# Kernel optimization log

Hardware: AMD Instinct MI355X
Metric: run time of the kernel (lower is better)

Reference implementation:

```python
import math
import jax, jax.numpy as jnp
import numpy as np

OLEN = 512
RATIO = 0.5
DROP_P = 0.2


def _gat(x, src, dst, W, a_s, a_d, b):
    """PyG GATConv (heads=1, concat=True, add_self_loops=True, neg_slope=0.2)."""
    n = x.shape[0]
    loops = jnp.arange(n, dtype=src.dtype)
    s = jnp.concatenate([src, loops])  # [E+N] source nodes
    d = jnp.concatenate([dst, loops])  # [E+N] destination nodes
    h = x @ W                           # [N, H]
    alpha_s = h @ a_s                   # [N]
    alpha_d = h @ a_d                   # [N]
    e = jax.nn.leaky_relu(alpha_s[s] + alpha_d[d], 0.2)  # [E+N]
    # segment softmax over destination neighborhoods
    m = jax.ops.segment_max(e, d, num_segments=n)
    ee = jnp.exp(e - m[d])
    denom = jax.ops.segment_sum(ee, d, num_segments=n)
    alpha = ee / denom[d]
    out = jax.ops.segment_sum(alpha[:, None] * h[s], d, num_segments=n)
    return out + b


def _forward(x, src, dst, W1, a_src1, a_dst1, b1, W2, a_src2, a_dst2, b2,
             W3, a_src3, a_dst3, b3, W_rel, W_root, b_pool):
    N, E = x.shape[0], src.shape[0]
    key = jax.random.key(42)
    h = x
    for i, (W, a_s, a_d, b) in enumerate([(W1, a_src1, a_dst1, b1),
                                          (W2, a_src2, a_dst2, b2),
                                          (W3, a_src3, a_dst3, b3)]):
        h = jax.nn.relu(_gat(h, src, dst, W, a_s, a_d, b))
        keep = jax.random.bernoulli(jax.random.fold_in(key, i), 1.0 - DROP_P, h.shape)
        h = jnp.where(keep, h / (1.0 - DROP_P), 0.0)  # F.dropout(training=True)

    # SAGPooling(GraphConv score, ratio=0.5, tanh) repeated until n <= 512.
    # Node counts are static per iteration (k = ceil(0.5*n)); edge arrays keep
    # fixed size E with a validity mask (edges dropped when an endpoint is pooled away).
    cur_src, cur_dst = src, dst
    emask = jnp.ones((E,), dtype=h.dtype)
    n = N
    while True:
        agg = jax.ops.segment_sum(h[cur_src] * emask[:, None], cur_dst, num_segments=n)
        score = (agg @ W_rel + h @ W_root + b_pool)[:, 0]  # GraphConv(d->1), aggr='add'
        score = jnp.tanh(score)
        k = math.ceil(RATIO * n)
        top_vals, perm = jax.lax.top_k(score, k)
        h = h[perm] * top_vals[:, None]
        inv = jnp.full((n,), -1, dtype=cur_src.dtype).at[perm].set(
            jnp.arange(k, dtype=cur_src.dtype))
        ns, nd = inv[cur_src], inv[cur_dst]
        valid = (ns >= 0) & (nd >= 0)
        emask = emask * valid.astype(emask.dtype)
        cur_src = jnp.where(valid, ns, 0)
        cur_dst = jnp.where(valid, nd, 0)
        n = k
        if n <= OLEN:
            break

    out = jnp.zeros((OLEN, h.shape[1]), h.dtype).at[:n].set(h)
    return out


def setup_inputs() -> dict:
    key = jax.random.key(0)
    ks = jax.random.split(key, 20)
    N, E, IDIM, HDIM = 50000, 800000, 128, 200
    inp = {
        "x": jax.random.normal(ks[0], (N, IDIM), jnp.float32),
        "src": jax.random.randint(ks[1], (E,), 0, N, jnp.int32),
        "dst": jax.random.randint(ks[2], (E,), 0, N, jnp.int32),
    }
    def w(k, shape, fan_in):
        return jax.random.normal(k, shape, jnp.float32) / np.sqrt(fan_in).astype(np.float32)
    inp["W1"] = w(ks[3], (IDIM, HDIM), IDIM)
    inp["a_src1"] = w(ks[4], (HDIM,), HDIM)
    inp["a_dst1"] = w(ks[5], (HDIM,), HDIM)
    inp["b1"] = jnp.zeros((HDIM,), jnp.float32)
    inp["W2"] = w(ks[6], (HDIM, HDIM), HDIM)
    inp["a_src2"] = w(ks[7], (HDIM,), HDIM)
    inp["a_dst2"] = w(ks[8], (HDIM,), HDIM)
    inp["b2"] = jnp.zeros((HDIM,), jnp.float32)
    inp["W3"] = w(ks[9], (HDIM, HDIM), HDIM)
    inp["a_src3"] = w(ks[10], (HDIM,), HDIM)
    inp["a_dst3"] = w(ks[11], (HDIM,), HDIM)
    inp["b3"] = jnp.zeros((HDIM,), jnp.float32)
    inp["W_rel"] = w(ks[12], (HDIM, 1), HDIM)
    inp["W_root"] = w(ks[13], (HDIM, 1), HDIM)
    inp["b_pool"] = jnp.zeros((1,), jnp.float32)
    return inp


def reference(x, src, dst, W1, a_src1, a_dst1, b1, W2, a_src2, a_dst2, b2,
              W3, a_src3, a_dst3, b3, W_rel, W_root, b_pool):
    return _forward(x, src, dst, W1, a_src1, a_dst1, b1, W2, a_src2, a_dst2, b2,
                    W3, a_src3, a_dst3, b3, W_rel, W_root, b_pool)
```

## Files before the change

kernel.cpp:

```cpp
#include <hip/hip_runtime.h>
#include <cstdint>
#include <cstddef>


__host__ __device__ inline void tf_round(uint32_t &x0, uint32_t &x1, int r) {
  x0 += x1;
  x1 = (x1 << r) | (x1 >> (32 - r));
  x1 ^= x0;
}

__host__ __device__ inline void threefry2x32(uint32_t k0, uint32_t k1,
                                             uint32_t &x0, uint32_t &x1) {
  uint32_t ks2 = k0 ^ k1 ^ 0x1BD11BDAu;
  x0 += k0; x1 += k1;
  tf_round(x0, x1, 13); tf_round(x0, x1, 15); tf_round(x0, x1, 26); tf_round(x0, x1, 6);
  x0 += k1; x1 += ks2 + 1u;
  tf_round(x0, x1, 17); tf_round(x0, x1, 29); tf_round(x0, x1, 16); tf_round(x0, x1, 24);
  x0 += ks2; x1 += k0 + 2u;
  tf_round(x0, x1, 13); tf_round(x0, x1, 15); tf_round(x0, x1, 26); tf_round(x0, x1, 6);
  x0 += k0; x1 += k1 + 3u;
  tf_round(x0, x1, 17); tf_round(x0, x1, 29); tf_round(x0, x1, 16); tf_round(x0, x1, 24);
  x0 += k1; x1 += ks2 + 4u;
  tf_round(x0, x1, 13); tf_round(x0, x1, 15); tf_round(x0, x1, 26); tf_round(x0, x1, 6);
  x0 += ks2; x1 += k0 + 5u;
}

__global__ __launch_bounds__(256) void gemm200_k(
    const float* __restrict__ A, const float* __restrict__ B,
    float* __restrict__ C, int M, int K) {
  __shared__ __align__(16) float As[128 * 8];
  __shared__ __align__(16) float Bs[8][208];
  int tid = threadIdx.x;
  int m0 = blockIdx.x * 128;
  int r = tid >> 2;
  int colBase = (tid & 3) * 52;
  float acc0[52], acc1[52];
#pragma unroll
  for (int q = 0; q < 52; q++) { acc0[q] = 0.f; acc1[q] = 0.f; }

  for (int k0 = 0; k0 < K; k0 += 8) {
    {
      int row = tid >> 1;
      int c = (tid & 1) * 4;
      int gm = m0 + row;
      float4 v = make_float4(0.f, 0.f, 0.f, 0.f);
      if (gm < M) v = *(const float4*)(A + (size_t)gm * K + (k0 + c));
      *(float4*)(&As[row * 8 + c]) = v;
    }
    for (int t = tid; t < 400; t += 256) {
      int kk = t / 50;
      int c = (t - kk * 50) * 4;
      *(float4*)(&Bs[kk][c]) = *(const float4*)(B + (size_t)(k0 + kk) * 200 + c);
    }
    __syncthreads();
#pragma unroll
    for (int kk = 0; kk < 8; kk++) {
      float a0 = As[r * 8 + kk];
      float a1 = As[(r + 64) * 8 + kk];
#pragma unroll
      for (int q = 0; q < 13; q++) {
        float4 b = *(const float4*)(&Bs[kk][colBase + 4 * q]);
        acc0[4 * q + 0] += a0 * b.x; acc0[4 * q + 1] += a0 * b.y;
        acc0[4 * q + 2] += a0 * b.z; acc0[4 * q + 3] += a0 * b.w;
        acc1[4 * q + 0] += a1 * b.x; acc1[4 * q + 1] += a1 * b.y;
        acc1[4 * q + 2] += a1 * b.z; acc1[4 * q + 3] += a1 * b.w;
      }
    }
    __syncthreads();
  }
  int gm0 = m0 + r, gm1 = m0 + r + 64;
#pragma unroll
  for (int q = 0; q < 52; q++) {
    int col = colBase + q;
    if (col < 200) {
      if (gm0 < M) C[(size_t)gm0 * 200 + col] = acc0[q];
      if (gm1 < M) C[(size_t)gm1 * 200 + col] = acc1[q];
    }
  }
}

__global__ __launch_bounds__(256) void dual_dot_k(
    const float* __restrict__ H, const float* __restrict__ v1,
    const float* __restrict__ v2, float* __restrict__ o1,
    float* __restrict__ o2, int n) {
  int wave = blockIdx.x * 4 + (threadIdx.x >> 6);
  int lane = threadIdx.x & 63;
  if (wave >= n) return;
  const float* row = H + (size_t)wave * 200;
  float s1 = 0.f, s2 = 0.f;
  for (int d = lane; d < 200; d += 64) {
    float h = row[d];
    s1 += h * v1[d];
    s2 += h * v2[d];
  }
  for (int off = 32; off; off >>= 1) {
    s1 += __shfl_down(s1, off);
    s2 += __shfl_down(s2, off);
  }
  if (lane == 0) { o1[wave] = s1; o2[wave] = s2; }
}

__global__ __launch_bounds__(256) void indeg_k(const int* __restrict__ dst,
                                               int* __restrict__ cnt, int E) {
  int e = blockIdx.x * 256 + threadIdx.x;
  if (e < E) atomicAdd(&cnt[dst[e]], 1);
}

__global__ __launch_bounds__(256) void scan_k(const int* __restrict__ cnt,
                                              int* __restrict__ rowptr, int N) {
  __shared__ int psum[256];
  int t = threadIdx.x;
  int CH = (N + 255) / 256;
  int beg = t * CH, end = min(beg + CH, N);
  if (beg > N) { beg = N; }
  int s = 0;
  for (int i = beg; i < end; i++) s += cnt[i];
  psum[t] = s;
  __syncthreads();
  if (t == 0) {
    int run = 0;
    for (int i = 0; i < 256; i++) { int v = psum[i]; psum[i] = run; run += v; }
  }
  __syncthreads();
  int run = psum[t];
  for (int i = beg; i < end; i++) { rowptr[i] = run; run += cnt[i]; }
  if (end == N && beg <= N) rowptr[N] = run;
}

__global__ __launch_bounds__(256) void cpyint_k(const int* __restrict__ a,
                                                int* __restrict__ b, int n) {
  int i = blockIdx.x * 256 + threadIdx.x;
  if (i < n) b[i] = a[i];
}

__global__ __launch_bounds__(256) void place_k(const int* __restrict__ dst,
                                               int* __restrict__ curs,
                                               int* __restrict__ csr, int E) {
  int e = blockIdx.x * 256 + threadIdx.x;
  if (e >= E) return;
  int pos = atomicAdd(&curs[dst[e]], 1);
  csr[pos] = e;
}

__global__ __launch_bounds__(256) void sortrow_k(const int* __restrict__ rowptr,
                                                 int* __restrict__ csr, int N) {
  int d = blockIdx.x * 256 + threadIdx.x;
  if (d >= N) return;
  int b = rowptr[d], e2 = rowptr[d + 1];
  for (int i = b + 1; i < e2; i++) {
    int v = csr[i];
    int j = i - 1;
    while (j >= b && csr[j] > v) { csr[j + 1] = csr[j]; j--; }
    csr[j + 1] = v;
  }
}

__device__ inline float dec_ord(unsigned enc) {
  unsigned b = (enc & 0x80000000u) ? (enc ^ 0x80000000u) : ~enc;
  return __uint_as_float(b);
}

__global__ __launch_bounds__(256) void edge_max_k(
    const int* __restrict__ src, const int* __restrict__ dst,
    const float* __restrict__ as_, const float* __restrict__ ad_,
    unsigned* __restrict__ menc, int E, int N) {
  int j = blockIdx.x * 256 + threadIdx.x;
  if (j >= E + N) return;
  int s, d;
  if (j < E) { s = src[j]; d = dst[j]; } else { s = j - E; d = s; }
  float v = as_[s] + ad_[d];
  float ev = (v >= 0.f) ? v : 0.2f * v;
  unsigned b = __float_as_uint(ev);
  unsigned enc = (b & 0x80000000u) ? ~b : (b | 0x80000000u);
  atomicMax(&menc[d], enc);
}

__global__ __launch_bounds__(256) void ee_k(
    const int* __restrict__ src, const int* __restrict__ dst,
    const float* __restrict__ as_, const float* __restrict__ ad_,
    const unsigned* __restrict__ menc, float* __restrict__ ee, int E, int N) {
  int j = blockIdx.x * 256 + threadIdx.x;
  if (j >= E + N) return;
  int s, d;
  if (j < E) { s = src[j]; d = dst[j]; } else { s = j - E; d = s; }
  float v = as_[s] + ad_[d];
  float ev = (v >= 0.f) ? v : 0.2f * v;
  ee[j] = expf(ev - dec_ord(menc[d]));
}

__global__ __launch_bounds__(256) void den_k(const int* __restrict__ rowptr,
                                             const int* __restrict__ csr,
                                             const float* __restrict__ ee,
                                             float* __restrict__ den, int E, int N) {
  int d = blockIdx.x * 256 + threadIdx.x;
  if (d >= N) return;
  float s = 0.f;
  int b = rowptr[d], e2 = rowptr[d + 1];
  for (int i = b; i < e2; i++) s = __fadd_rn(s, ee[csr[i]]);
  s = __fadd_rn(s, ee[E + d]);
  den[d] = s;
}

__global__ __launch_bounds__(256) void alpha_k(const int* __restrict__ dst,
                                               const float* __restrict__ den,
                                               float* __restrict__ ee, int E, int N) {
  int j = blockIdx.x * 256 + threadIdx.x;
  if (j >= E + N) return;
  int d = (j < E) ? dst[j] : (j - E);
  ee[j] = ee[j] / den[d];
}

__global__ __launch_bounds__(256) void gat_out_k(
    const int* __restrict__ rowptr, const int* __restrict__ csr,
    const int* __restrict__ src, const float* __restrict__ alpha,
    const float* __restrict__ HW, float* __restrict__ OUT, int E, int N) {
  int node = blockIdx.x * 4 + (threadIdx.x >> 6);
  int lane = threadIdx.x & 63;
  if (node >= N || lane >= 50) return;
  int b = rowptr[node];
  int deg = rowptr[node + 1] - b;
  int cnt = deg + 1;

  auto fetchS = [&](int t, int &s, float &w) {
    if (t < deg) {
      int e = csr[b + t];
      s = src[e];
      w = alpha[e];
    } else if (t == deg) {
      s = node;
      w = alpha[E + node];
    } else {
      s = node;
      w = 0.f;
    }
  };

  int s0, s1, s2;
  float w0, w1, w2;
  fetchS(0, s0, w0);
  fetchS(1, s1, w1);
  fetchS(2, s2, w2);
  float4 h0 = *(const float4*)(HW + (size_t)s0 * 200 + 4 * lane);
  float4 h1 = *(const float4*)(HW + (size_t)s1 * 200 + 4 * lane);
  float4 acc = make_float4(0.f, 0.f, 0.f, 0.f);
  for (int t = 0; t < cnt; t++) {
    int s3;
    float w3;
    fetchS(t + 3, s3, w3);
    float4 h2 = *(const float4*)(HW + (size_t)s2 * 200 + 4 * lane);
    acc.x = __fadd_rn(acc.x, __fmul_rn(w0, h0.x));
    acc.y = __fadd_rn(acc.y, __fmul_rn(w0, h0.y));
    acc.z = __fadd_rn(acc.z, __fmul_rn(w0, h0.z));
    acc.w = __fadd_rn(acc.w, __fmul_rn(w0, h0.w));
    h0 = h1; h1 = h2;
    w0 = w1; w1 = w2; w2 = w3;
    s2 = s3;
  }
  *(float4*)(OUT + (size_t)node * 200 + 4 * lane) = acc;
}

__global__ __launch_bounds__(256) void epi_k(float* __restrict__ H,
                                             const float* __restrict__ bias,
                                             uint32_t k0, uint32_t k1, int total) {
  int t = blockIdx.x * 256 + threadIdx.x;
  if (t >= total) return;
  uint32_t x0 = 0u, x1 = (uint32_t)t;
  threefry2x32(k0, k1, x0, x1);
  uint32_t bits = x0 ^ x1;
  float u = __uint_as_float((bits >> 9) | 0x3f800000u) - 1.0f;
  int col = t % 200;
  float v = H[t] + bias[col];
  v = fmaxf(v, 0.f);
  H[t] = (u < 0.8f) ? (v / 0.8f) : 0.f;
}

__global__ __launch_bounds__(256) void einit_k(
    const int* __restrict__ src, const int* __restrict__ dst,
    int* __restrict__ cs, int* __restrict__ cd, int* __restrict__ orig,
    int E, int N) {
  int e = blockIdx.x * 256 + threadIdx.x;
  if (e < E) { cs[e] = src[e]; cd[e] = dst[e]; }
  if (e < N) orig[e] = e;
}

__global__ __launch_bounds__(256) void pool_agg_k(
    const int* __restrict__ rowptr, const int* __restrict__ csr,
    const int* __restrict__ csrc, const int* __restrict__ orig,
    const float* __restrict__ H, float* __restrict__ AGG, int n) {
  int node = blockIdx.x * 4 + (threadIdx.x >> 6);
  int lane = threadIdx.x & 63;
  if (node >= n || lane >= 50) return;
  int o = orig[node];
  int b = rowptr[o];
  int deg = rowptr[o + 1] - b;

  auto fetchS = [&](int t, int &s, float &w) {
    if (t < deg) {
      int e = csr[b + t];
      int sv = csrc[e];
      s = (sv >= 0) ? sv : 0;
      w = (sv >= 0) ? 1.f : 0.f;
    } else {
      s = 0;
      w = 0.f;
    }
  };

  int s0, s1, s2;
  float w0, w1, w2;
  fetchS(0, s0, w0);
  fetchS(1, s1, w1);
  fetchS(2, s2, w2);
  float4 h0 = *(const float4*)(H + (size_t)s0 * 200 + 4 * lane);
  float4 h1 = *(const float4*)(H + (size_t)s1 * 200 + 4 * lane);
  float4 acc = make_float4(0.f, 0.f, 0.f, 0.f);
  for (int t = 0; t < deg; t++) {
    int s3;
    float w3;
    fetchS(t + 3, s3, w3);
    float4 h2 = *(const float4*)(H + (size_t)s2 * 200 + 4 * lane);
    acc.x = __fadd_rn(acc.x, __fmul_rn(w0, h0.x));
    acc.y = __fadd_rn(acc.y, __fmul_rn(w0, h0.y));
    acc.z = __fadd_rn(acc.z, __fmul_rn(w0, h0.z));
    acc.w = __fadd_rn(acc.w, __fmul_rn(w0, h0.w));
    h0 = h1; h1 = h2;
    w0 = w1; w1 = w2; w2 = w3;
    s2 = s3;
  }
  *(float4*)(AGG + (size_t)node * 200 + 4 * lane) = acc;
}

__global__ __launch_bounds__(256) void score2_k(
    const float* __restrict__ AGG, const float* __restrict__ H,
    const float* __restrict__ wrel, const float* __restrict__ wroot,
    const float* __restrict__ bp, float* __restrict__ score, int n) {
  int node = blockIdx.x * 4 + (threadIdx.x >> 6);
  int lane = threadIdx.x & 63;
  if (node >= n) return;
  const float* arow = AGG + (size_t)node * 200;
  const float* hrow = H + (size_t)node * 200;
  float s1 = 0.f, s2 = 0.f;
  for (int d = lane; d < 200; d += 64) {
    s1 += arow[d] * wrel[d];
    s2 += hrow[d] * wroot[d];
  }
  for (int off = 32; off; off >>= 1) {
    s1 += __shfl_down(s1, off);
    s2 += __shfl_down(s2, off);
  }
  if (lane == 0) score[node] = tanhf((s1 + s2) + bp[0]);
}

__global__ __launch_bounds__(256) void renc_k(const float* __restrict__ score,
                                              unsigned* __restrict__ keyA,
                                              int* __restrict__ payA, int n) {
  int i = blockIdx.x * 256 + threadIdx.x;
  if (i >= n) return;
  unsigned b = __float_as_uint(score[i]);
  if (b == 0x80000000u) b = 0u;
  unsigned enc = (b & 0x80000000u) ? ~b : (b | 0x80000000u);
  keyA[i] = ~enc;
  payA[i] = i;
}

__global__ __launch_bounds__(256) void rhist_k(const unsigned* __restrict__ key,
                                               int* __restrict__ counts,
                                               int n, int NB, int shift) {
  __shared__ int hist[256];
  hist[threadIdx.x] = 0;
  __syncthreads();
  int i = blockIdx.x * 256 + threadIdx.x;
  if (i < n) atomicAdd(&hist[(key[i] >> shift) & 255u], 1);
  __syncthreads();
  counts[threadIdx.x * NB + blockIdx.x] = hist[threadIdx.x];
}

__global__ __launch_bounds__(256) void rscan_k(const int* __restrict__ counts,
                                               int* __restrict__ base, int NB) {
  __shared__ int tot[256];
  int t = threadIdx.x;
  int s = 0;
  for (int b = 0; b < NB; b++) s += counts[t * NB + b];
  tot[t] = s;
  __syncthreads();
  if (t == 0) {
    int run = 0;
    for (int i = 0; i < 256; i++) { int v = tot[i]; tot[i] = run; run += v; }
  }
  __syncthreads();
  int run = tot[t];
  for (int b = 0; b < NB; b++) { base[t * NB + b] = run; run += counts[t * NB + b]; }
}

__global__ __launch_bounds__(256) void rscatter_k(
    const unsigned* __restrict__ keyIn, const int* __restrict__ payIn,
    const int* __restrict__ base, unsigned* __restrict__ keyOut,
    int* __restrict__ payOut, int n, int NB, int shift) {
  __shared__ int dig[256];
  int t = threadIdx.x;
  int i = blockIdx.x * 256 + t;
  unsigned k = 0u;
  int p = 0, d = -1;
  if (i < n) {
    k = keyIn[i];
    p = payIn[i];
    d = (int)((k >> shift) & 255u);
  }
  dig[t] = d;
  __syncthreads();
  if (i < n) {
    int local = 0;
    for (int j = 0; j < t; j++) local += (dig[j] == d) ? 1 : 0;
    int pos = base[d * NB + blockIdx.x] + local;
    keyOut[pos] = k;
    payOut[pos] = p;
  }
}

__global__ __launch_bounds__(256) void ranksort_k(const int* __restrict__ pay,
                                                  int* __restrict__ perm,
                                                  int* __restrict__ inv,
                                                  int n, int k) {
  int r = blockIdx.x * 256 + threadIdx.x;
  if (r >= n) return;
  int i = pay[r];
  if (r < k) { perm[r] = i; inv[i] = r; }
  else inv[i] = -1;
}

__global__ __launch_bounds__(256) void orig_update_k(const int* __restrict__ perm,
                                                     const int* __restrict__ oin,
                                                     int* __restrict__ oout, int k) {
  int r = blockIdx.x * 256 + threadIdx.x;
  if (r < k) oout[r] = oin[perm[r]];
}

__global__ __launch_bounds__(256) void gather_k(
    const float* __restrict__ H, const int* __restrict__ perm,
    const float* __restrict__ score, float* __restrict__ Ho, int k) {
  int r = blockIdx.x;
  int d = threadIdx.x;
  int p = perm[r];
  float s = score[p];
  if (d < 200) Ho[(size_t)r * 200 + d] = __fmul_rn(H[(size_t)p * 200 + d], s);
}

__global__ __launch_bounds__(256) void remap_k(int* __restrict__ cs,
                                               int* __restrict__ cd,
                                               const int* __restrict__ inv, int E) {
  int e = blockIdx.x * 256 + threadIdx.x;
  if (e >= E) return;
  int a = cs[e];
  if (a < 0) return;
  int na = inv[a], nb = inv[cd[e]];
  bool valid = (na >= 0) && (nb >= 0);
  cs[e] = valid ? na : -1;
  cd[e] = valid ? nb : -1;
}

__global__ __launch_bounds__(256) void out_copy_k(const float* __restrict__ h,
                                                  float* __restrict__ out, int cnt) {
  int t = blockIdx.x * 256 + threadIdx.x;
  if (t < cnt) out[t] = h[t];
}

extern "C" void kernel_launch(void* const* d_in, const int* in_sizes, int n_in,
                              void* d_out, int out_size, void* d_ws, size_t ws_size,
                              hipStream_t stream) {
  const int ID = 128, HD = 200;
  const int N = in_sizes[0] / ID;
  const int E = in_sizes[1];
  const int ET = E + N;
  const int total = N * HD;

  const float* x = (const float*)d_in[0];
  const int* src = (const int*)d_in[1];
  const int* dst = (const int*)d_in[2];
  const float* W[3]   = {(const float*)d_in[3], (const float*)d_in[7], (const float*)d_in[11]};
  const float* asv[3] = {(const float*)d_in[4], (const float*)d_in[8], (const float*)d_in[12]};
  const float* adv[3] = {(const float*)d_in[5], (const float*)d_in[9], (const float*)d_in[13]};
  const float* bv[3]  = {(const float*)d_in[6], (const float*)d_in[10], (const float*)d_in[14]};
  const float* Wrel  = (const float*)d_in[15];
  const float* Wroot = (const float*)d_in[16];
  const float* bpool = (const float*)d_in[17];

  char* ws = (char*)d_ws;
  float*    bufA  = (float*)(ws + 0);
  float*    bufB  = (float*)(ws + 40000000);
  float*    as_   = (float*)(ws + 80000000);
  float*    ad_   = (float*)(ws + 80200000);
  float*    ee_   = (float*)(ws + 80400000);
  unsigned* menc  = (unsigned*)(ws + 83800000);
  float*    den   = (float*)(ws + 84000000);
  float*    score = (float*)(ws + 84200000);
  int*      rank_ = (int*)(ws + 84400000);
  int*      perm_ = (int*)(ws + 84600000);
  int*      inv_  = (int*)(ws + 84800000);
  int*      origA = (int*)(ws + 85000000);
  int*      origB = (int*)(ws + 85200000);
  int*      rowptr= (int*)(ws + 85400000);
  int*      curs  = (int*)(ws + 85650000);
  int*      csr   = (int*)(ws + 85850000);
  int*      csrc  = (int*)(ws + 89050000);
  int*      cdst  = (int*)(ws + 92250000);

  char* rx = ws + 80400000;
  unsigned* keyA   = (unsigned*)(rx + 0 * 262144);
  unsigned* keyB   = (unsigned*)(rx + 1 * 262144);
  int*      payA   = (int*)(rx + 2 * 262144);
  int*      payB   = (int*)(rx + 3 * 262144);
  int*      rcounts= (int*)(rx + 4 * 262144);
  int*      rbase  = (int*)(rx + 5 * 262144);

  uint32_t fk0[3], fk1[3];
  for (int i = 0; i < 3; i++) {
    uint32_t a = 0u, b = (uint32_t)i;
    threefry2x32(0u, 42u, a, b);
    fk0[i] = a; fk1[i] = b;
  }

  const int B256 = 256;
  hipMemsetAsync(rank_, 0, (size_t)N * 4, stream);
  indeg_k<<<(E + 255) / 256, B256, 0, stream>>>(dst, rank_, E);
  scan_k<<<1, B256, 0, stream>>>(rank_, rowptr, N);
  cpyint_k<<<(N + 255) / 256, B256, 0, stream>>>(rowptr, curs, N);
  place_k<<<(E + 255) / 256, B256, 0, stream>>>(dst, curs, csr, E);
  sortrow_k<<<(N + 255) / 256, B256, 0, stream>>>(rowptr, csr, N);

  for (int i = 0; i < 3; i++) {
    const float* in = (i == 0) ? x : bufB;
    int K = (i == 0) ? ID : HD;
    gemm200_k<<<(N + 127) / 128, B256, 0, stream>>>(in, W[i], bufA, N, K);
    dual_dot_k<<<(N + 3) / 4, B256, 0, stream>>>(bufA, asv[i], adv[i], as_, ad_, N);
    hipMemsetAsync(menc, 0, (size_t)N * 4, stream);
    edge_max_k<<<(ET + 255) / 256, B256, 0, stream>>>(src, dst, as_, ad_, menc, E, N);
    ee_k<<<(ET + 255) / 256, B256, 0, stream>>>(src, dst, as_, ad_, menc, ee_, E, N);
    den_k<<<(N + 255) / 256, B256, 0, stream>>>(rowptr, csr, ee_, den, E, N);
    alpha_k<<<(ET + 255) / 256, B256, 0, stream>>>(dst, den, ee_, E, N);
    gat_out_k<<<(N + 3) / 4, B256, 0, stream>>>(rowptr, csr, src, ee_, bufA, bufB, E, N);
    epi_k<<<(total + 255) / 256, B256, 0, stream>>>(bufB, bv[i], fk0[i], fk1[i], total);
  }

  einit_k<<<(E + 255) / 256, B256, 0, stream>>>(src, dst, csrc, cdst, origA, E, N);
  float* hcur = bufB;
  float* hnext = bufA;
  int* ocur = origA;
  int* onext = origB;
  int n = N;
  while (true) {
    int k = (n + 1) / 2;
    int NB = (n + 255) / 256;
    pool_agg_k<<<(n + 3) / 4, B256, 0, stream>>>(rowptr, csr, csrc, ocur, hcur, hnext, n);
    score2_k<<<(n + 3) / 4, B256, 0, stream>>>(hnext, hcur, Wrel, Wroot, bpool, score, n);
    renc_k<<<NB, B256, 0, stream>>>(score, keyA, payA, n);
    unsigned* ki = keyA; unsigned* ko = keyB;
    int* pi = payA; int* po = payB;
    for (int pass = 0; pass < 4; pass++) {
      int shift = pass * 8;
      rhist_k<<<NB, B256, 0, stream>>>(ki, rcounts, n, NB, shift);
      rscan_k<<<1, B256, 0, stream>>>(rcounts, rbase, NB);
      rscatter_k<<<NB, B256, 0, stream>>>(ki, pi, rbase, ko, po, n, NB, shift);
      { unsigned* t = ki; ki = ko; ko = t; }
      { int* t = pi; pi = po; po = t; }
    }
    ranksort_k<<<NB, B256, 0, stream>>>(pi, perm_, inv_, n, k);
    orig_update_k<<<(k + 255) / 256, B256, 0, stream>>>(perm_, ocur, onext, k);
    gather_k<<<k, B256, 0, stream>>>(hcur, perm_, score, hnext, k);
    remap_k<<<(E + 255) / 256, B256, 0, stream>>>(csrc, cdst, inv_, E);
    { float* t = hcur; hcur = hnext; hnext = t; }
    { int* t = ocur; ocur = onext; onext = t; }
    n = k;
    if (n <= 512) break;
  }

  hipMemsetAsync(d_out, 0, (size_t)out_size * 4, stream);
  out_copy_k<<<(n * HD + 255) / 256, B256, 0, stream>>>(hcur, (float*)d_out, n * HD);
}
```

Baseline: 3.055 ms.

## Prefetch GEMM tiles into registers, vectorize stores, and fuse radix sort stages

The GEMM now loads the next A/B k-slice into registers while computing the current one, pads the A shared tile to stride 9 to avoid bank conflicts, and writes results with float4 stores. The pooling top-k radix sort fuses key encoding with the first histogram, and fuses the final scatter with the perm/inv construction and orig-index update. This removes several kernel launches per pooling iteration and some global round trips. Register pressure in the GEMM rises from holding the prefetched tiles.

```diff
diff --git a/kernel.cpp b/kernel.cpp
--- a/kernel.cpp
+++ b/kernel.cpp
@@ -28,35 +28,50 @@
 __global__ __launch_bounds__(256) void gemm200_k(
     const float* __restrict__ A, const float* __restrict__ B,
     float* __restrict__ C, int M, int K) {
-  __shared__ __align__(16) float As[128 * 8];
+  __shared__ float As[128 * 9];
   __shared__ __align__(16) float Bs[8][208];
   int tid = threadIdx.x;
   int m0 = blockIdx.x * 128;
   int r = tid >> 2;
   int colBase = (tid & 3) * 52;
+  int nq = (colBase == 156) ? 11 : 13;
   float acc0[52], acc1[52];
 #pragma unroll
   for (int q = 0; q < 52; q++) { acc0[q] = 0.f; acc1[q] = 0.f; }
 
+  int arow = tid >> 1;
+  int ac = (tid & 1) * 4;
+  int gmA = m0 + arow;
+  const float* Aptr = A + (size_t)gmA * K + ac;
+  int bk0 = tid / 50, bc0 = (tid - bk0 * 50) * 4;
+  int t2 = tid + 256;
+  int bk1 = t2 / 50, bc1 = (t2 - bk1 * 50) * 4;
+  bool hasB1 = (t2 < 400);
+
+  float4 va = make_float4(0.f, 0.f, 0.f, 0.f);
+  if (gmA < M) va = *(const float4*)(Aptr);
+  float4 vb0 = *(const float4*)(B + (size_t)bk0 * 200 + bc0);
+  float4 vb1 = make_float4(0.f, 0.f, 0.f, 0.f);
+  if (hasB1) vb1 = *(const float4*)(B + (size_t)bk1 * 200 + bc1);
+
   for (int k0 = 0; k0 < K; k0 += 8) {
-    {
-      int row = tid >> 1;
-      int c = (tid & 1) * 4;
-      int gm = m0 + row;
-      float4 v = make_float4(0.f, 0.f, 0.f, 0.f);
-      if (gm < M) v = *(const float4*)(A + (size_t)gm * K + (k0 + c));
-      *(float4*)(&As[row * 8 + c]) = v;
+    As[arow * 9 + ac + 0] = va.x;
+    As[arow * 9 + ac + 1] = va.y;
+    As[arow * 9 + ac + 2] = va.z;
+    As[arow * 9 + ac + 3] = va.w;
+    *(float4*)(&Bs[bk0][bc0]) = vb0;
+    if (hasB1) *(float4*)(&Bs[bk1][bc1]) = vb1;
+    __syncthreads();
+    int kn = k0 + 8;
+    if (kn < K) {
+      if (gmA < M) va = *(const float4*)(Aptr + kn);
+      vb0 = *(const float4*)(B + (size_t)(kn + bk0) * 200 + bc0);
+      if (hasB1) vb1 = *(const float4*)(B + (size_t)(kn + bk1) * 200 + bc1);
     }
-    for (int t = tid; t < 400; t += 256) {
-      int kk = t / 50;
-      int c = (t - kk * 50) * 4;
-      *(float4*)(&Bs[kk][c]) = *(const float4*)(B + (size_t)(k0 + kk) * 200 + c);
-    }
-    __syncthreads();
 #pragma unroll
     for (int kk = 0; kk < 8; kk++) {
-      float a0 = As[r * 8 + kk];
-      float a1 = As[(r + 64) * 8 + kk];
+      float a0 = As[r * 9 + kk];
+      float a1 = As[(r + 64) * 9 + kk];
 #pragma unroll
       for (int q = 0; q < 13; q++) {
         float4 b = *(const float4*)(&Bs[kk][colBase + 4 * q]);
@@ -70,11 +85,15 @@
   }
   int gm0 = m0 + r, gm1 = m0 + r + 64;
 #pragma unroll
-  for (int q = 0; q < 52; q++) {
-    int col = colBase + q;
-    if (col < 200) {
-      if (gm0 < M) C[(size_t)gm0 * 200 + col] = acc0[q];
-      if (gm1 < M) C[(size_t)gm1 * 200 + col] = acc1[q];
+  for (int q = 0; q < 13; q++) {
+    if (q < nq) {
+      int col = colBase + 4 * q;
+      float4 v0 = make_float4(acc0[4 * q + 0], acc0[4 * q + 1],
+                              acc0[4 * q + 2], acc0[4 * q + 3]);
+      float4 v1 = make_float4(acc1[4 * q + 0], acc1[4 * q + 1],
+                              acc1[4 * q + 2], acc1[4 * q + 3]);
+      if (gm0 < M) *(float4*)(C + (size_t)gm0 * 200 + col) = v0;
+      if (gm1 < M) *(float4*)(C + (size_t)gm1 * 200 + col) = v1;
     }
   }
 }
@@ -351,16 +370,27 @@
   if (lane == 0) score[node] = tanhf((s1 + s2) + bp[0]);
 }
 
-__global__ __launch_bounds__(256) void renc_k(const float* __restrict__ score,
-                                              unsigned* __restrict__ keyA,
-                                              int* __restrict__ payA, int n) {
+
+__global__ __launch_bounds__(256) void rhenc_k(const float* __restrict__ score,
+                                               unsigned* __restrict__ keyA,
+                                               int* __restrict__ payA,
+                                               int* __restrict__ counts,
+                                               int n, int NB) {
+  __shared__ int hist[256];
+  hist[threadIdx.x] = 0;
+  __syncthreads();
   int i = blockIdx.x * 256 + threadIdx.x;
-  if (i >= n) return;
-  unsigned b = __float_as_uint(score[i]);
-  if (b == 0x80000000u) b = 0u;
-  unsigned enc = (b & 0x80000000u) ? ~b : (b | 0x80000000u);
-  keyA[i] = ~enc;
-  payA[i] = i;
+  if (i < n) {
+    unsigned b = __float_as_uint(score[i]);
+    if (b == 0x80000000u) b = 0u;
+    unsigned enc = (b & 0x80000000u) ? ~b : (b | 0x80000000u);
+    unsigned key = ~enc;
+    keyA[i] = key;
+    payA[i] = i;
+    atomicAdd(&hist[key & 255u], 1);
+  }
+  __syncthreads();
+  counts[threadIdx.x * NB + blockIdx.x] = hist[threadIdx.x];
 }
 
 __global__ __launch_bounds__(256) void rhist_k(const unsigned* __restrict__ key,
@@ -417,22 +447,28 @@
   }
 }
 
-__global__ __launch_bounds__(256) void ranksort_k(const int* __restrict__ pay,
-                                                  int* __restrict__ perm,
-                                                  int* __restrict__ inv,
-                                                  int n, int k) {
-  int r = blockIdx.x * 256 + threadIdx.x;
-  if (r >= n) return;
-  int i = pay[r];
-  if (r < k) { perm[r] = i; inv[i] = r; }
-  else inv[i] = -1;
-}
-
-__global__ __launch_bounds__(256) void orig_update_k(const int* __restrict__ perm,
-                                                     const int* __restrict__ oin,
-                                                     int* __restrict__ oout, int k) {
-  int r = blockIdx.x * 256 + threadIdx.x;
-  if (r < k) oout[r] = oin[perm[r]];
+__global__ __launch_bounds__(256) void rscatterF_k(
+    const unsigned* __restrict__ keyIn, const int* __restrict__ payIn,
+    const int* __restrict__ base, const int* __restrict__ oin,
+    int* __restrict__ oout, int* __restrict__ perm, int* __restrict__ inv,
+    int n, int NB, int k) {
+  __shared__ int dig[256];
+  int t = threadIdx.x;
+  int i = blockIdx.x * 256 + t;
+  int p = 0, d = -1;
+  if (i < n) {
+    p = payIn[i];
+    d = (int)((keyIn[i] >> 24) & 255u);
+  }
+  dig[t] = d;
+  __syncthreads();
+  if (i < n) {
+    int local = 0;
+    for (int j = 0; j < t; j++) local += (dig[j] == d) ? 1 : 0;
+    int pos = base[d * NB + blockIdx.x] + local;
+    if (pos < k) { perm[pos] = p; inv[p] = pos; oout[pos] = oin[p]; }
+    else inv[p] = -1;
+  }
 }
 
 __global__ __launch_bounds__(256) void gather_k(
@@ -552,19 +588,19 @@
     int NB = (n + 255) / 256;
     pool_agg_k<<<(n + 3) / 4, B256, 0, stream>>>(rowptr, csr, csrc, ocur, hcur, hnext, n);
     score2_k<<<(n + 3) / 4, B256, 0, stream>>>(hnext, hcur, Wrel, Wroot, bpool, score, n);
-    renc_k<<<NB, B256, 0, stream>>>(score, keyA, payA, n);
-    unsigned* ki = keyA; unsigned* ko = keyB;
-    int* pi = payA; int* po = payB;
-    for (int pass = 0; pass < 4; pass++) {
-      int shift = pass * 8;
-      rhist_k<<<NB, B256, 0, stream>>>(ki, rcounts, n, NB, shift);
-      rscan_k<<<1, B256, 0, stream>>>(rcounts, rbase, NB);
-      rscatter_k<<<NB, B256, 0, stream>>>(ki, pi, rbase, ko, po, n, NB, shift);
-      { unsigned* t = ki; ki = ko; ko = t; }
-      { int* t = pi; pi = po; po = t; }
-    }
-    ranksort_k<<<NB, B256, 0, stream>>>(pi, perm_, inv_, n, k);
-    orig_update_k<<<(k + 255) / 256, B256, 0, stream>>>(perm_, ocur, onext, k);
+    rhenc_k<<<NB, B256, 0, stream>>>(score, keyA, payA, rcounts, n, NB);
+    rscan_k<<<1, B256, 0, stream>>>(rcounts, rbase, NB);
+    rscatter_k<<<NB, B256, 0, stream>>>(keyA, payA, rbase, keyB, payB, n, NB, 0);
+    rhist_k<<<NB, B256, 0, stream>>>(keyB, rcounts, n, NB, 8);
+    rscan_k<<<1, B256, 0, stream>>>(rcounts, rbase, NB);
+    rscatter_k<<<NB, B256, 0, stream>>>(keyB, payB, rbase, keyA, payA, n, NB, 8);
+    rhist_k<<<NB, B256, 0, stream>>>(keyA, rcounts, n, NB, 16);
+    rscan_k<<<1, B256, 0, stream>>>(rcounts, rbase, NB);
+    rscatter_k<<<NB, B256, 0, stream>>>(keyA, payA, rbase, keyB, payB, n, NB, 16);
+    rhist_k<<<NB, B256, 0, stream>>>(keyB, rcounts, n, NB, 24);
+    rscan_k<<<1, B256, 0, stream>>>(rcounts, rbase, NB);
+    rscatterF_k<<<NB, B256, 0, stream>>>(keyB, payB, rbase, ocur, onext, perm_, inv_,
+                                         n, NB, k);
     gather_k<<<k, B256, 0, stream>>>(hcur, perm_, score, hnext, k);
     remap_k<<<(E + 255) / 256, B256, 0, stream>>>(csrc, cdst, inv_, E);
     { float* t = hcur; hcur = hnext; hnext = t; }
```

After: 2.625 ms. 14.1% less time.
